# Performance work log

Hardware: AMD Instinct MI355X
Metric: run time of the kernel (lower is better)

Reference implementation:

```python
import jax, jax.numpy as jnp
import numpy as np
import itertools

# The repo's eset_ops_4_to_4 builds 69 permutation-equivariant basis ops on a
# rank-4 set tensor x[n, d, i, j, k, l]. We reconstruct the 69-dim basis as all
# order-preserving subset matchings (A, B) with A = kept input index slots,
# B = output slots receiving them (|A| = |B| = s, s = 1..4): sum x over the
# complement of A, then broadcast the reduced tensor into output positions B.
# Count: sum_{s=1..4} C(4,s)^2 = 16 + 36 + 16 + 1 = 69 (Vandermonde C(8,4)=70
# minus the s=0 global-sum term).

def _basis_pairs():
    pairs = []
    for s in range(1, 5):
        for A in itertools.combinations(range(4), s):
            for B in itertools.combinations(range(4), s):
                pairs.append((A, B))
    return pairs  # len == 69

_PAIRS = _basis_pairs()


def _forward(x, coefs, bias):
    # x: (n, d, N, N, N, N); coefs: (d, s_out, 69); bias: (1, s_out, 1,1,1,1)
    out_shape = (x.shape[0], coefs.shape[1]) + x.shape[2:]
    out = jnp.zeros(out_shape, x.dtype)
    for idx, (A, B) in enumerate(_PAIRS):
        sum_axes = tuple(2 + i for i in range(4) if i not in A)
        red = x.sum(axis=sum_axes) if sum_axes else x  # (n, d, N^|A|)
        # mix channels on the SMALL reduced tensor (op and channel mix commute)
        term = jnp.einsum('ds,nd...->ns...', coefs[:, :, idx], red)
        # place kept axes at output slots B (order-preserving), broadcast rest
        for p in range(4):
            if p not in B:
                term = jnp.expand_dims(term, axis=2 + p)
        out = out + term  # broadcasting add == broadcast then accumulate
    return out + bias


def setup_inputs() -> dict:
    key = jax.random.key(0)
    k1, k2 = jax.random.split(key)
    n, d, s_out, N, basis = 2, 8, 8, 32, 69
    x = jax.random.normal(k1, (n, d, N, N, N, N), dtype=jnp.float32)
    std = np.sqrt(2.0 / (d + s_out + basis)).astype(np.float32)
    coefs = std * jax.random.normal(k2, (d, s_out, basis), dtype=jnp.float32)
    bias = jnp.zeros((1, s_out, 1, 1, 1, 1), dtype=jnp.float32)
    return {'x': x, 'coefs': coefs, 'bias': bias}


def reference(x, coefs, bias):
    return _forward(x, coefs, bias)
```

## Files before the change

kernel.cpp:

```cpp
#include <hip/hip_runtime.h>


constexpr size_t R3SZ  = 524288;
constexpr size_t R2SZ  = 16384;
constexpr size_t R1SZ  = 512;
constexpr size_t R3OFF = 0;
constexpr size_t R2OFF = R3OFF + 4 * R3SZ;
constexpr size_t R1OFF = R2OFF + 6 * R2SZ;
constexpr size_t T2OFF = R1OFF + 4 * R1SZ;
constexpr size_t T1OFF = T2OFF + 6 * R2SZ;
constexpr size_t U3OFF = T1OFF + 4 * R1SZ;

__global__ __launch_bounds__(256) void k_plane(const float* __restrict__ x,
                                               float* __restrict__ ws) {
    __shared__ float4 cp[4][8];
    __shared__ float b012[256];
    __shared__ float b013[256];
    const int bid = blockIdx.x;
    const int jq = bid & 3;
    const int i  = (bid >> 2) & 31;
    const int nd = bid >> 7;
    const int t  = threadIdx.x;
    const int w  = t >> 6;
    const int lane = t & 63;
    const float* xp = x + ((size_t)nd << 20) + ((size_t)i << 15) + (size_t)jq * 8192;

    #pragma unroll
    for (int jj = 0; jj < 8; ++jj) {
        float4 v = *(const float4*)(xp + jj * 1024 + t * 4);
        float h = v.x + v.y + v.z + v.w;
        h += __shfl_xor(h, 1); h += __shfl_xor(h, 2); h += __shfl_xor(h, 4);
        if ((t & 7) == 0) b012[jj * 32 + (t >> 3)] = h;
        v.x += __shfl_xor(v.x, 8);  v.y += __shfl_xor(v.y, 8);
        v.z += __shfl_xor(v.z, 8);  v.w += __shfl_xor(v.w, 8);
        v.x += __shfl_xor(v.x, 16); v.y += __shfl_xor(v.y, 16);
        v.z += __shfl_xor(v.z, 16); v.w += __shfl_xor(v.w, 16);
        v.x += __shfl_xor(v.x, 32); v.y += __shfl_xor(v.y, 32);
        v.z += __shfl_xor(v.z, 32); v.w += __shfl_xor(v.w, 32);
        if (lane < 8) cp[w][lane] = v;
        __syncthreads();
        if (t < 8) {
            float4 s0 = cp[0][t], s1 = cp[1][t], s2 = cp[2][t], s3 = cp[3][t];
            float4 s;
            s.x = s0.x + s1.x + s2.x + s3.x;
            s.y = s0.y + s1.y + s2.y + s3.y;
            s.z = s0.z + s1.z + s2.z + s3.z;
            s.w = s0.w + s1.w + s2.w + s3.w;
            *(float4*)(&b013[jj * 32 + t * 4]) = s;
        }
        __syncthreads();
    }
    const size_t base = ((size_t)nd << 15) + ((size_t)i << 10) + jq * 256;
    ws[R3OFF + base + t]         = b012[t];
    ws[R3OFF + R3SZ + base + t]  = b013[t];
}

__global__ __launch_bounds__(256) void k_col(const float* __restrict__ x,
                                             float* __restrict__ ws) {
    const int b = blockIdx.x;
    const int t = threadIdx.x;
    if (b < 512) {
        const int i  = b & 31;
        const int nd = b >> 5;
        const float* xp = x + ((size_t)nd << 20) + ((size_t)i << 15) + t * 4;
        float4 acc = {0.f, 0.f, 0.f, 0.f};
        #pragma unroll 8
        for (int j = 0; j < 32; ++j) {
            float4 v = *(const float4*)(xp + j * 1024);
            acc.x += v.x; acc.y += v.y; acc.z += v.z; acc.w += v.w;
        }
        *(float4*)(ws + R3OFF + 2 * R3SZ + ((size_t)nd << 15) + ((size_t)i << 10)
                   + t * 4) = acc;
    } else {
        const int bb = b - 512;
        const int j  = bb & 31;
        const int nd = bb >> 5;
        const float* xp = x + ((size_t)nd << 20) + (size_t)j * 1024 + t * 4;
        float4 acc = {0.f, 0.f, 0.f, 0.f};
        #pragma unroll 8
        for (int i = 0; i < 32; ++i) {
            float4 v = *(const float4*)(xp + ((size_t)i << 15));
            acc.x += v.x; acc.y += v.y; acc.z += v.z; acc.w += v.w;
        }
        *(float4*)(ws + R3OFF + 3 * R3SZ + ((size_t)nd << 15) + ((size_t)j << 10)
                   + t * 4) = acc;
    }
}

__global__ __launch_bounds__(256) void k_red21(float* __restrict__ ws) {
    const int gid = blockIdx.x * 256 + threadIdx.x;
    if (gid < 98304) {
        const int b2 = gid >> 14;
        const int r  = gid & 16383;
        const int nd = r >> 10;
        const int p = (r >> 5) & 31, q = r & 31;
        const float* r012 = ws + R3OFF + ((size_t)nd << 15);
        const float* r013 = r012 + R3SZ;
        const float* r023 = r012 + 2 * R3SZ;
        float s = 0.f;
        switch (b2) {
            case 0: { const float* s0 = r012 + p * 1024 + q * 32;
                      for (int m = 0; m < 32; ++m) s += s0[m]; } break;
            case 1: { const float* s0 = r012 + p * 1024 + q;
                      for (int m = 0; m < 32; ++m) s += s0[m * 32]; } break;
            case 2: { const float* s0 = r013 + p * 1024 + q;
                      for (int m = 0; m < 32; ++m) s += s0[m * 32]; } break;
            case 3: { const float* s0 = r012 + p * 32 + q;
                      for (int m = 0; m < 32; ++m) s += s0[m * 1024]; } break;
            case 4: { const float* s0 = r013 + p * 32 + q;
                      for (int m = 0; m < 32; ++m) s += s0[m * 1024]; } break;
            default:{ const float* s0 = r023 + p * 32 + q;
                      for (int m = 0; m < 32; ++m) s += s0[m * 1024]; } break;
        }
        ws[R2OFF + (size_t)b2 * R2SZ + (size_t)nd * 1024 + p * 32 + q] = s;
    } else if (gid < 100352) {
        const int e  = gid - 98304;
        const int b1 = e >> 9;
        const int r  = e & 511;
        const int nd = r >> 5, p = r & 31;
        const float* r012 = ws + R3OFF + ((size_t)nd << 15);
        const float* r013 = r012 + R3SZ;
        float s = 0.f;
        if (b1 == 0)      { const float* s0 = r012 + p * 1024;
                            for (int m = 0; m < 1024; ++m) s += s0[m]; }
        else if (b1 == 1) { const float* s0 = r012 + p * 32;
                            for (int a = 0; a < 32; ++a) for (int m = 0; m < 32; ++m)
                                s += s0[a * 1024 + m]; }
        else if (b1 == 2) { const float* s0 = r012 + p;
                            for (int a = 0; a < 32; ++a) for (int m = 0; m < 32; ++m)
                                s += s0[a * 1024 + m * 32]; }
        else              { const float* s0 = r013 + p;
                            for (int a = 0; a < 32; ++a) for (int m = 0; m < 32; ++m)
                                s += s0[a * 1024 + m * 32]; }
        ws[R1OFF + (size_t)b1 * R1SZ + (size_t)nd * 32 + p] = s;
    }
}

__global__ __launch_bounds__(256) void k_mix21(const float* __restrict__ coefs,
                                               float* __restrict__ ws) {
    __shared__ float cs[4416];
    for (int idx = threadIdx.x; idx < 4416; idx += 256) cs[idx] = coefs[idx];
    __syncthreads();
    const int gid = blockIdx.x * 256 + threadIdx.x;
    if (gid < 98304) {
        const int b2 = gid >> 14;
        const int r  = gid & 16383;
        const int n  = r >> 13;
        const int so = (r >> 10) & 7;
        const int pq = r & 1023;
        float s = 0.f;
        #pragma unroll
        for (int a2 = 0; a2 < 6; ++a2) {
            const float* src = ws + R2OFF + (size_t)a2 * R2SZ + (size_t)(n * 8) * 1024 + pq;
            #pragma unroll
            for (int d = 0; d < 8; ++d)
                s += cs[(d * 8 + so) * 69 + 16 + a2 * 6 + b2] * src[d * 1024];
        }
        ws[T2OFF + (size_t)b2 * R2SZ + (size_t)(n * 8 + so) * 1024 + pq] = s;
    } else if (gid < 100352) {
        const int e  = gid - 98304;
        const int b1 = e >> 9;
        const int r  = e & 511;
        const int n  = r >> 8;
        const int so = (r >> 5) & 7;
        const int p  = r & 31;
        float s = 0.f;
        #pragma unroll
        for (int a1 = 0; a1 < 4; ++a1) {
            const float* src = ws + R1OFF + (size_t)a1 * R1SZ + (size_t)(n * 8) * 32 + p;
            #pragma unroll
            for (int d = 0; d < 8; ++d)
                s += cs[(d * 8 + so) * 69 + a1 * 4 + b1] * src[d * 32];
        }
        ws[T1OFF + (size_t)b1 * R1SZ + (size_t)(n * 8 + so) * 32 + p] = s;
    }
}

__global__ __launch_bounds__(256) void k_mix3(const float* __restrict__ coefs,
                                              const float* __restrict__ bias,
                                              float* __restrict__ ws) {
    __shared__ float cs[4416];
    for (int idx = threadIdx.x; idx < 4416; idx += 256) cs[idx] = coefs[idx];
    __syncthreads();
    const int blk = blockIdx.x;
    const int cb  = blk & 127;
    const int soh = (blk >> 7) & 1;
    const int n   = blk >> 8;
    const int c   = cb * 256 + threadIdx.x;
    const int p1 = c >> 10, p2 = (c >> 5) & 31, p3 = c & 31;
    float v[4][8];
    #pragma unroll
    for (int a = 0; a < 4; ++a)
        #pragma unroll
        for (int d = 0; d < 8; ++d)
            v[a][d] = ws[R3OFF + (size_t)a * R3SZ + (size_t)(n * 8 + d) * 32768 + c];
    const float* T2 = ws + T2OFF;
    const float* T1 = ws + T1OFF;
    #pragma unroll
    for (int b = 0; b < 4; ++b) {
        #pragma unroll
        for (int so2 = 0; so2 < 4; ++so2) {
            const int so = soh * 4 + so2;
            float s = 0.f;
            #pragma unroll
            for (int a = 0; a < 4; ++a)
                #pragma unroll
                for (int d = 0; d < 8; ++d)
                    s += cs[(d * 8 + so) * 69 + 52 + a * 4 + b] * v[a][d];
            const size_t nso = (size_t)(n * 8 + so);
            if (b == 0) {
                s += T2[0 * R2SZ + nso * 1024 + p1 * 32 + p2];
                s += T2[1 * R2SZ + nso * 1024 + p1 * 32 + p3];
                s += T2[3 * R2SZ + nso * 1024 + p2 * 32 + p3];
                s += T1[0 * R1SZ + nso * 32 + p1];
                s += T1[1 * R1SZ + nso * 32 + p2];
                s += T1[2 * R1SZ + nso * 32 + p3];
                s += bias[so];
            } else if (b == 1) {
                s += T2[2 * R2SZ + nso * 1024 + p1 * 32 + p3];
                s += T2[4 * R2SZ + nso * 1024 + p2 * 32 + p3];
                s += T1[3 * R1SZ + nso * 32 + p3];
            } else if (b == 2) {
                s += T2[5 * R2SZ + nso * 1024 + p2 * 32 + p3];
            }
            ws[U3OFF + (size_t)b * R3SZ + nso * 32768 + c] = s;
        }
    }
}

__global__ __launch_bounds__(256) void k_final(const float* __restrict__ x,
                                               const float* __restrict__ coefs,
                                               const float* __restrict__ ws,
                                               float* __restrict__ out) {
    __shared__ float c68[64];
    if (threadIdx.x < 64) c68[threadIdx.x] = coefs[threadIdx.x * 69 + 68];
    __syncthreads();
    const int b = blockIdx.x;
    const int j = b & 31;
    const int i = (b >> 5) & 31;
    const int n = b >> 10;
    const int t = threadIdx.x;
    const int k = t >> 3, lq = t & 7;

    float4 xv[8];
    const float* xb = x + ((size_t)n << 23) + ((size_t)i << 15) + j * 1024 + k * 32 + lq * 4;
    #pragma unroll
    for (int d = 0; d < 8; ++d) xv[d] = *(const float4*)(xb + ((size_t)d << 20));

    const float* U = ws + U3OFF;
    const size_t c012 = (size_t)i * 1024 + j * 32 + k;
    const size_t c013 = (size_t)i * 1024 + j * 32 + lq * 4;
    const size_t c023 = (size_t)i * 1024 + k * 32 + lq * 4;
    const size_t c123 = (size_t)j * 1024 + k * 32 + lq * 4;

    #pragma unroll
    for (int so = 0; so < 8; ++so) {
        const size_t nso = (size_t)(n * 8 + so) << 15;
        const float  u0 = U[0 * R3SZ + nso + c012];
        const float4 u1 = *(const float4*)(U + 1 * R3SZ + nso + c013);
        const float4 u2 = *(const float4*)(U + 2 * R3SZ + nso + c023);
        const float4 u3 = *(const float4*)(U + 3 * R3SZ + nso + c123);
        float4 acc;
        acc.x = u0 + u1.x + u2.x + u3.x;
        acc.y = u0 + u1.y + u2.y + u3.y;
        acc.z = u0 + u1.z + u2.z + u3.z;
        acc.w = u0 + u1.w + u2.w + u3.w;
        #pragma unroll
        for (int d = 0; d < 8; ++d) {
            const float w = c68[d * 8 + so];
            acc.x += w * xv[d].x; acc.y += w * xv[d].y;
            acc.z += w * xv[d].z; acc.w += w * xv[d].w;
        }
        *(float4*)(out + ((size_t)(n * 8 + so) << 20) + ((size_t)i << 15)
                   + j * 1024 + k * 32 + lq * 4) = acc;
    }
}

extern "C" void kernel_launch(void* const* d_in, const int* in_sizes, int n_in,
                              void* d_out, int out_size, void* d_ws, size_t ws_size,
                              hipStream_t stream) {
    const float* x     = (const float*)d_in[0];
    const float* coefs = (const float*)d_in[1];
    const float* bias  = (const float*)d_in[2];
    float* out = (float*)d_out;
    float* ws  = (float*)d_ws;

    hipLaunchKernelGGL(k_plane, dim3(2048), dim3(256), 0, stream, x, ws);
    hipLaunchKernelGGL(k_col,   dim3(1024), dim3(256), 0, stream, x, ws);
    hipLaunchKernelGGL(k_red21, dim3(392),  dim3(256), 0, stream, ws);
    hipLaunchKernelGGL(k_mix21, dim3(392),  dim3(256), 0, stream, coefs, ws);
    hipLaunchKernelGGL(k_mix3,  dim3(512),  dim3(256), 0, stream, coefs, bias, ws);
    hipLaunchKernelGGL(k_final, dim3(2048), dim3(256), 0, stream, x, coefs, ws, out);
}
```

Measured before the change: 201.8 us.

## Fuse plane and column reductions into one kernel sharing x reads

Merges k_plane and the first half of k_col into a single k_red3 kernel. Each 512-thread block reads a full i-slab of x once and produces the r012, r013 and r023 reductions from the same loads, with the j loop split across two half-blocks that are combined through shared memory. The remaining column reduction (r123) is also folded into this launch. The aim is to drop one full pass over x (128 MB total) and one launch, at the cost of higher shared-memory use (~20 KB) and lower occupancy per block.

```diff
diff --git a/kernel.cpp b/kernel.cpp
--- a/kernel.cpp
+++ b/kernel.cpp
@@ -11,79 +11,79 @@
 constexpr size_t T1OFF = T2OFF + 6 * R2SZ;
 constexpr size_t U3OFF = T1OFF + 4 * R1SZ;
 
-__global__ __launch_bounds__(256) void k_plane(const float* __restrict__ x,
-                                               float* __restrict__ ws) {
-    __shared__ float4 cp[4][8];
-    __shared__ float b012[256];
-    __shared__ float b013[256];
-    const int bid = blockIdx.x;
-    const int jq = bid & 3;
-    const int i  = (bid >> 2) & 31;
-    const int nd = bid >> 7;
-    const int t  = threadIdx.x;
-    const int w  = t >> 6;
-    const int lane = t & 63;
-    const float* xp = x + ((size_t)nd << 20) + ((size_t)i << 15) + (size_t)jq * 8192;
-
-    #pragma unroll
-    for (int jj = 0; jj < 8; ++jj) {
-        float4 v = *(const float4*)(xp + jj * 1024 + t * 4);
-        float h = v.x + v.y + v.z + v.w;
-        h += __shfl_xor(h, 1); h += __shfl_xor(h, 2); h += __shfl_xor(h, 4);
-        if ((t & 7) == 0) b012[jj * 32 + (t >> 3)] = h;
-        v.x += __shfl_xor(v.x, 8);  v.y += __shfl_xor(v.y, 8);
-        v.z += __shfl_xor(v.z, 8);  v.w += __shfl_xor(v.w, 8);
-        v.x += __shfl_xor(v.x, 16); v.y += __shfl_xor(v.y, 16);
-        v.z += __shfl_xor(v.z, 16); v.w += __shfl_xor(v.w, 16);
-        v.x += __shfl_xor(v.x, 32); v.y += __shfl_xor(v.y, 32);
-        v.z += __shfl_xor(v.z, 32); v.w += __shfl_xor(v.w, 32);
-        if (lane < 8) cp[w][lane] = v;
+__global__ __launch_bounds__(512) void k_red3(const float* __restrict__ x,
+                                              float* __restrict__ ws) {
+    __shared__ float4 cp[32][4][8];
+    __shared__ float  b012[1024];
+    __shared__ float4 a2[256];
+    const int bid  = blockIdx.x;
+    const int t    = threadIdx.x;
+    const int half = t >> 8;
+    const int tt   = t & 255;
+    const int k    = tt >> 3;
+    const int l4   = tt & 7;
+
+    if (bid < 512) {
+        const int i    = bid & 31;
+        const int nd   = bid >> 5;
+        const int w4   = (t >> 6) & 3;
+        const int lane = t & 63;
+        const float* xp = x + ((size_t)nd << 20) + ((size_t)i << 15) + k * 32 + l4 * 4;
+        float4 acc = {0.f, 0.f, 0.f, 0.f};
+        #pragma unroll
+        for (int it = 0; it < 16; ++it) {
+            const int j = it * 2 + half;
+            float4 v = *(const float4*)(xp + j * 1024);
+            acc.x += v.x; acc.y += v.y; acc.z += v.z; acc.w += v.w;
+            float h = v.x + v.y + v.z + v.w;
+            h += __shfl_xor(h, 1); h += __shfl_xor(h, 2); h += __shfl_xor(h, 4);
+            if (l4 == 0) b012[j * 32 + k] = h;
+            v.x += __shfl_xor(v.x, 8);  v.y += __shfl_xor(v.y, 8);
+            v.z += __shfl_xor(v.z, 8);  v.w += __shfl_xor(v.w, 8);
+            v.x += __shfl_xor(v.x, 16); v.y += __shfl_xor(v.y, 16);
+            v.z += __shfl_xor(v.z, 16); v.w += __shfl_xor(v.w, 16);
+            v.x += __shfl_xor(v.x, 32); v.y += __shfl_xor(v.y, 32);
+            v.z += __shfl_xor(v.z, 32); v.w += __shfl_xor(v.w, 32);
+            if (lane < 8) cp[j][w4][lane] = v;
+        }
+        if (half == 1) a2[tt] = acc;
         __syncthreads();
-        if (t < 8) {
-            float4 s0 = cp[0][t], s1 = cp[1][t], s2 = cp[2][t], s3 = cp[3][t];
+        const size_t base = ((size_t)nd << 15) + ((size_t)i << 10);
+        *(float2*)(ws + R3OFF + base + 2 * t) = *(const float2*)(b012 + 2 * t);
+        if (half == 0) {
+            const int j = tt >> 3, lj = tt & 7;
+            float4 s0 = cp[j][0][lj], s1 = cp[j][1][lj];
+            float4 s2 = cp[j][2][lj], s3 = cp[j][3][lj];
             float4 s;
             s.x = s0.x + s1.x + s2.x + s3.x;
             s.y = s0.y + s1.y + s2.y + s3.y;
             s.z = s0.z + s1.z + s2.z + s3.z;
             s.w = s0.w + s1.w + s2.w + s3.w;
-            *(float4*)(&b013[jj * 32 + t * 4]) = s;
-        }
-        __syncthreads();
-    }
-    const size_t base = ((size_t)nd << 15) + ((size_t)i << 10) + jq * 256;
-    ws[R3OFF + base + t]         = b012[t];
-    ws[R3OFF + R3SZ + base + t]  = b013[t];
-}
-
-__global__ __launch_bounds__(256) void k_col(const float* __restrict__ x,
-                                             float* __restrict__ ws) {
-    const int b = blockIdx.x;
-    const int t = threadIdx.x;
-    if (b < 512) {
-        const int i  = b & 31;
-        const int nd = b >> 5;
-        const float* xp = x + ((size_t)nd << 20) + ((size_t)i << 15) + t * 4;
-        float4 acc = {0.f, 0.f, 0.f, 0.f};
-        #pragma unroll 8
-        for (int j = 0; j < 32; ++j) {
-            float4 v = *(const float4*)(xp + j * 1024);
-            acc.x += v.x; acc.y += v.y; acc.z += v.z; acc.w += v.w;
-        }
-        *(float4*)(ws + R3OFF + 2 * R3SZ + ((size_t)nd << 15) + ((size_t)i << 10)
-                   + t * 4) = acc;
+            *(float4*)(ws + R3OFF + R3SZ + base + j * 32 + lj * 4) = s;
+            float4 b = a2[tt];
+            acc.x += b.x; acc.y += b.y; acc.z += b.z; acc.w += b.w;
+            *(float4*)(ws + R3OFF + 2 * R3SZ + base + k * 32 + l4 * 4) = acc;
+        }
     } else {
-        const int bb = b - 512;
+        const int bb = bid - 512;
         const int j  = bb & 31;
         const int nd = bb >> 5;
-        const float* xp = x + ((size_t)nd << 20) + (size_t)j * 1024 + t * 4;
+        const float* xp = x + ((size_t)nd << 20) + (size_t)j * 1024 + (size_t)tt * 4;
         float4 acc = {0.f, 0.f, 0.f, 0.f};
-        #pragma unroll 8
-        for (int i = 0; i < 32; ++i) {
+        #pragma unroll
+        for (int it = 0; it < 16; ++it) {
+            const int i = it * 2 + half;
             float4 v = *(const float4*)(xp + ((size_t)i << 15));
             acc.x += v.x; acc.y += v.y; acc.z += v.z; acc.w += v.w;
         }
-        *(float4*)(ws + R3OFF + 3 * R3SZ + ((size_t)nd << 15) + ((size_t)j << 10)
-                   + t * 4) = acc;
+        if (half == 1) a2[tt] = acc;
+        __syncthreads();
+        if (half == 0) {
+            float4 b = a2[tt];
+            acc.x += b.x; acc.y += b.y; acc.z += b.z; acc.w += b.w;
+            *(float4*)(ws + R3OFF + 3 * R3SZ + ((size_t)nd << 15)
+                       + ((size_t)j << 10) + tt * 4) = acc;
+        }
     }
 }
 
@@ -285,8 +285,7 @@
     float* out = (float*)d_out;
     float* ws  = (float*)d_ws;
 
-    hipLaunchKernelGGL(k_plane, dim3(2048), dim3(256), 0, stream, x, ws);
-    hipLaunchKernelGGL(k_col,   dim3(1024), dim3(256), 0, stream, x, ws);
+    hipLaunchKernelGGL(k_red3, dim3(1024), dim3(512), 0, stream, x, ws);
     hipLaunchKernelGGL(k_red21, dim3(392),  dim3(256), 0, stream, ws);
     hipLaunchKernelGGL(k_mix21, dim3(392),  dim3(256), 0, stream, coefs, ws);
     hipLaunchKernelGGL(k_mix3,  dim3(512),  dim3(256), 0, stream, coefs, bias, ws);
```

Result: faster. 190.6 us (-5.6%).
